# Kernel tuning notes

Measured on AMD Instinct MI355X. Metric: run time of the kernel, lower is better.

## Reference

```python
import jax, jax.numpy as jnp
import numpy as np

D_MODEL = 512
N_HEADS = 8
D_K = D_MODEL // N_HEADS
LN_EPS = 1e-5


def setup_inputs() -> dict:
    key = jax.random.key(0)
    ks = jax.random.split(key, 8)
    B, S, D = 2, 4096, D_MODEL
    # xavier_uniform bound for square [D, D] weight
    bound = float(np.sqrt(6.0 / (D + D)))
    x = jax.random.normal(ks[0], (B, S, D), dtype=jnp.float32)
    w_q = jax.random.uniform(ks[1], (D, D), jnp.float32, -bound, bound)
    w_k = jax.random.uniform(ks[2], (D, D), jnp.float32, -bound, bound)
    w_v = jax.random.uniform(ks[3], (D, D), jnp.float32, -bound, bound)
    # w_o: torch Linear default init (kaiming-uniform-ish); uniform is fine as data
    lim = float(1.0 / np.sqrt(D))
    w_o = jax.random.uniform(ks[4], (D, D), jnp.float32, -lim, lim)
    b_o = jax.random.uniform(ks[5], (D,), jnp.float32, -lim, lim)
    ln_gamma = jnp.ones((D,), jnp.float32)
    ln_beta = jnp.zeros((D,), jnp.float32)
    return {"x": x, "w_q": w_q, "w_k": w_k, "w_v": w_v,
            "w_o": w_o, "b_o": b_o, "ln_gamma": ln_gamma, "ln_beta": ln_beta}


def _layer_norm(x, gamma, beta):
    mu = jnp.mean(x, axis=-1, keepdims=True)
    var = jnp.mean(jnp.square(x - mu), axis=-1, keepdims=True)
    return (x - mu) * jax.lax.rsqrt(var + LN_EPS) * gamma + beta


def reference(x, w_q, w_k, w_v, w_o, b_o, ln_gamma, ln_beta):
    B, S, D = x.shape
    residual = x
    h = _layer_norm(x, ln_gamma, ln_beta)
    # torch Linear: y = h @ W.T ; reshape to [B, H, S, d_k]
    def proj(W):
        return (h @ W.T).reshape(B, S, N_HEADS, D_K).transpose(0, 2, 1, 3)
    Q, K, V = proj(w_q), proj(w_k), proj(w_v)
    scores = jnp.einsum('bhqd,bhkd->bhqk', Q, K) / jnp.sqrt(jnp.float32(D_K))
    attn = jax.nn.softmax(scores, axis=-1)  # dropout p=0 -> identity
    attended = jnp.einsum('bhqk,bhkd->bhqd', attn, V)
    attended = attended.transpose(0, 2, 1, 3).reshape(B, S, D)
    out = attended @ w_o.T + b_o
    return out + residual
```

## Files before the change

kernel.cpp:

```cpp
#include <hip/hip_runtime.h>
#include <hip/hip_bf16.h>
#include <stdint.h>


typedef __bf16 bf16;
typedef __attribute__((ext_vector_type(8))) __bf16 bf16x8;
typedef __attribute__((ext_vector_type(4))) __bf16 bf16x4;
typedef __attribute__((ext_vector_type(4))) float f32x4;
typedef __attribute__((ext_vector_type(4))) unsigned int u32x4;

#define LOG2E 1.44269504088896340736f
#define SW(row, grp) (((row) << 6) + ((((grp) ^ ((row) & 7))) << 3))

__device__ __forceinline__ unsigned int pkbf16(float lo, float hi) {
  return __builtin_amdgcn_perm(__builtin_bit_cast(unsigned int, hi),
                               __builtin_bit_cast(unsigned int, lo),
                               0x07060302u);
}

__global__ __launch_bounds__(256) void ln_kernel(
    const float* __restrict__ x, const float* __restrict__ gamma,
    const float* __restrict__ beta, bf16* __restrict__ h) {
  int wave = threadIdx.x >> 6, lane = threadIdx.x & 63;
  int row = blockIdx.x * 4 + wave;
  const float* xr = x + (size_t)row * 512 + lane * 8;
  f32x4 v0 = *(const f32x4*)xr;
  f32x4 v1 = *(const f32x4*)(xr + 4);
  float f[8], s = 0.f, s2 = 0.f;
#pragma unroll
  for (int i = 0; i < 4; ++i) { f[i] = v0[i]; f[4 + i] = v1[i]; }
#pragma unroll
  for (int i = 0; i < 8; ++i) { s += f[i]; s2 += f[i] * f[i]; }
#pragma unroll
  for (int off = 1; off < 64; off <<= 1) {
    s  += __shfl_xor(s, off, 64);
    s2 += __shfl_xor(s2, off, 64);
  }
  float mu  = s * (1.f / 512.f);
  float var = s2 * (1.f / 512.f) - mu * mu;
  float rstd = rsqrtf(var + 1e-5f);
  f32x4 g0 = *(const f32x4*)(gamma + lane * 8);
  f32x4 g1 = *(const f32x4*)(gamma + lane * 8 + 4);
  f32x4 b0 = *(const f32x4*)(beta + lane * 8);
  f32x4 b1 = *(const f32x4*)(beta + lane * 8 + 4);
  bf16x8 o;
#pragma unroll
  for (int i = 0; i < 4; ++i) {
    o[i]     = (bf16)((f[i]     - mu) * rstd * g0[i] + b0[i]);
    o[4 + i] = (bf16)((f[4 + i] - mu) * rstd * g1[i] + b1[i]);
  }
  *(bf16x8*)(h + (size_t)row * 512 + lane * 8) = o;
}

__global__ __launch_bounds__(256) void qkv_kernel(
    const bf16* __restrict__ h, const float* __restrict__ wq,
    const float* __restrict__ wk, const float* __restrict__ wv,
    bf16* __restrict__ Qg, bf16* __restrict__ Kg, bf16* __restrict__ Vtg) {
  __shared__ bf16 As[128 * 64];
  __shared__ bf16 Bs[128 * 64];
  int tid = threadIdx.x, wave = tid >> 6, lane = tid & 63;
  int wm = wave >> 1, wn = wave & 1, quad = lane >> 4, l15 = lane & 15;
  int mtile = blockIdx.x;
  int wsel = blockIdx.y >> 2;
  int nb = blockIdx.y & 3;
  const float* W = (wsel == 0) ? wq : (wsel == 1 ? wk : wv);
  const bf16*  Abase = h + (size_t)mtile * 128 * 512;
  const float* Bbase = W + (size_t)nb * 128 * 512;
  f32x4 acc[4][4];
#pragma unroll
  for (int i = 0; i < 4; ++i)
#pragma unroll
    for (int j = 0; j < 4; ++j) acc[i][j] = (f32x4){0.f, 0.f, 0.f, 0.f};

  int srow = tid >> 3, grp = tid & 7, scol = grp * 8;
  bf16x8 ar[4];
  f32x4 br0[4], br1[4];
#pragma unroll
  for (int k = 0; k < 4; ++k) {
    int rr = srow + k * 32;
    ar[k]  = *(const bf16x8*)(Abase + (size_t)rr * 512 + scol);
    br0[k] = *(const f32x4*)(Bbase + (size_t)rr * 512 + scol);
    br1[k] = *(const f32x4*)(Bbase + (size_t)rr * 512 + scol + 4);
  }
  for (int k0 = 0; k0 < 512; k0 += 64) {
#pragma unroll
    for (int k = 0; k < 4; ++k) {
      int rr = srow + k * 32;
      int w = SW(rr, grp);
      *(bf16x8*)(As + w) = ar[k];
      bf16x8 wb;
#pragma unroll
      for (int j = 0; j < 4; ++j) { wb[j] = (bf16)br0[k][j]; wb[4 + j] = (bf16)br1[k][j]; }
      *(bf16x8*)(Bs + w) = wb;
    }
    __syncthreads();
    if (k0 < 448) {
#pragma unroll
      for (int k = 0; k < 4; ++k) {
        int rr = srow + k * 32;
        ar[k]  = *(const bf16x8*)(Abase + (size_t)rr * 512 + k0 + 64 + scol);
        br0[k] = *(const f32x4*)(Bbase + (size_t)rr * 512 + k0 + 64 + scol);
        br1[k] = *(const f32x4*)(Bbase + (size_t)rr * 512 + k0 + 64 + scol + 4);
      }
    }
#pragma unroll
    for (int c = 0; c < 2; ++c) {
      bf16x8 af[4], bw[4];
#pragma unroll
      for (int mt = 0; mt < 4; ++mt)
        af[mt] = *(const bf16x8*)(As + SW(wm * 64 + mt * 16 + l15, c * 4 + quad));
#pragma unroll
      for (int nt = 0; nt < 4; ++nt)
        bw[nt] = *(const bf16x8*)(Bs + SW(wn * 64 + nt * 16 + l15, c * 4 + quad));
#pragma unroll
      for (int mt = 0; mt < 4; ++mt)
#pragma unroll
        for (int nt = 0; nt < 4; ++nt)
          acc[mt][nt] = __builtin_amdgcn_mfma_f32_16x16x32_bf16(
              bw[nt], af[mt], acc[mt][nt], 0, 0, 0);
    }
    __syncthreads();
  }
  float qscale = (wsel == 0) ? (0.125f * LOG2E) : 1.0f;
#pragma unroll
  for (int mt = 0; mt < 4; ++mt) {
    int m_g = mtile * 128 + wm * 64 + mt * 16 + l15;
    int b = m_g >> 12, s = m_g & 4095;
#pragma unroll
    for (int nt = 0; nt < 4; ++nt) {
      int n_g = nb * 128 + wn * 64 + nt * 16 + quad * 4;
      int head = n_g >> 6, d = n_g & 63;
      f32x4 a = acc[mt][nt];
      if (wsel < 2) {
        bf16* dst = (wsel == 0 ? Qg : Kg) +
                    ((size_t)((b * 8 + head) * 4096 + s)) * 64 + d;
        bf16x4 pk;
#pragma unroll
        for (int r = 0; r < 4; ++r) pk[r] = (bf16)(a[r] * qscale);
        *(bf16x4*)dst = pk;
      } else {
        bf16* dst = Vtg + ((size_t)((b * 8 + head) * 64 + d)) * 4096 + s;
#pragma unroll
        for (int r = 0; r < 4; ++r) dst[(size_t)r * 4096] = (bf16)a[r];
      }
    }
  }
}

__global__ __launch_bounds__(256, 2) void attn_kernel(
    const bf16* __restrict__ Qg, const bf16* __restrict__ Kg,
    const bf16* __restrict__ Vtg, bf16* __restrict__ Og) {
  __shared__ char smem[64 * 1024];
  bf16* KV = (bf16*)smem;
  float* OL = (float*)smem;
  float* Ll = (float*)(smem + 49152);

  int tid = threadIdx.x, wave = tid >> 6, lane = tid & 63;
  int quad = lane >> 4, l15 = lane & 15;
  int qgrp = wave & 1, khalf = wave >> 1;
  int lin = blockIdx.x;
  int bh = ((lin & 7) << 1) | ((lin >> 3) & 1);
  int q0 = (lin >> 4) * 128;
  int hi = bh & 7, bi = bh >> 3;
  const bf16* Kh  = Kg  + (size_t)bh * 4096 * 64;
  const bf16* Vth = Vtg + (size_t)bh * 64 * 4096;

  bf16x8 qf[4][2];
#pragma unroll
  for (int mt = 0; mt < 4; ++mt)
#pragma unroll
    for (int c = 0; c < 2; ++c)
      qf[mt][c] = *(const bf16x8*)(
          Qg + ((size_t)bh * 4096 + q0 + qgrp * 64 + mt * 16 + l15) * 64 +
          c * 32 + quad * 8);

  f32x4 o_acc[4][4], lacc[4];
#pragma unroll
  for (int mt = 0; mt < 4; ++mt) {
    lacc[mt] = (f32x4){0.f, 0.f, 0.f, 0.f};
#pragma unroll
    for (int nt = 0; nt < 4; ++nt) o_acc[mt][nt] = (f32x4){0.f, 0.f, 0.f, 0.f};
  }
  const u32x4 onesu = {0x3F803F80u, 0x3F803F80u, 0x3F803F80u, 0x3F803F80u};
  const bf16x8 ones8 = __builtin_bit_cast(bf16x8, onesu);

  bf16* sbase = KV + khalf * 8192 + (qgrp ? 4096 : 0);
  bf16x8 sr[8];
  int key0 = khalf * 2048;
#pragma unroll
  for (int i = 0; i < 8; ++i) {
    int e = i * 512 + lane * 8;
    sr[i] = qgrp
        ? *(const bf16x8*)(Vth + (size_t)(e >> 6) * 4096 + key0 + (e & 63))
        : *(const bf16x8*)(Kh + (size_t)key0 * 64 + e);
  }
#pragma unroll
  for (int i = 0; i < 8; ++i) {
    int e = i * 512 + lane * 8;
    *(bf16x8*)(sbase + SW(e >> 6, (e >> 3) & 7)) = sr[i];
  }
#pragma unroll
  for (int i = 0; i < 8; ++i) {
    int e = i * 512 + lane * 8;
    sr[i] = qgrp
        ? *(const bf16x8*)(Vth + (size_t)(e >> 6) * 4096 + key0 + 64 + (e & 63))
        : *(const bf16x8*)(Kh + (size_t)(key0 + 64) * 64 + e);
  }
  __syncthreads();

  for (int kt = 0; kt < 32; ++kt) {
    int cur = kt & 1, nxt = cur ^ 1;
    bf16* Ksw = KV + cur * 16384 + khalf * 8192;
    bf16* Vsw = Ksw + 4096;
    if (kt < 31) {
#pragma unroll
      for (int i = 0; i < 8; ++i) {
        int e = i * 512 + lane * 8;
        *(bf16x8*)(sbase + nxt * 16384 + SW(e >> 6, (e >> 3) & 7)) = sr[i];
      }
    }
    if (kt < 30) {
      int kbase = key0 + (kt + 2) * 64;
#pragma unroll
      for (int i = 0; i < 8; ++i) {
        int e = i * 512 + lane * 8;
        sr[i] = qgrp
            ? *(const bf16x8*)(Vth + (size_t)(e >> 6) * 4096 + kbase + (e & 63))
            : *(const bf16x8*)(Kh + (size_t)kbase * 64 + e);
      }
    }
    bf16x8 kf[8];
#pragma unroll
    for (int kb = 0; kb < 4; ++kb)
#pragma unroll
      for (int c = 0; c < 2; ++c)
        kf[kb * 2 + c] = *(const bf16x8*)(Ksw + SW(kb * 16 + l15, c * 4 + quad));
    bf16x8 vf8[2][4];
#pragma unroll
    for (int pr = 0; pr < 2; ++pr)
#pragma unroll
      for (int nt = 0; nt < 4; ++nt) {
        bf16x4 lo = *(const bf16x4*)(
            &Vsw[SW(nt * 16 + l15, (pr * 2) * 2 + (quad >> 1)) + (quad & 1) * 4]);
        bf16x4 hi4 = *(const bf16x4*)(
            &Vsw[SW(nt * 16 + l15, (pr * 2 + 1) * 2 + (quad >> 1)) + (quad & 1) * 4]);
        bf16x8 v;
#pragma unroll
        for (int j = 0; j < 4; ++j) { v[j] = lo[j]; v[4 + j] = hi4[j]; }
        vf8[pr][nt] = v;
      }
#pragma unroll
    for (int mt = 0; mt < 4; ++mt) {
      f32x4 st[4];
#pragma unroll
      for (int kb = 0; kb < 4; ++kb) st[kb] = (f32x4){0.f, 0.f, 0.f, 0.f};
#pragma unroll
      for (int c = 0; c < 2; ++c)
#pragma unroll
        for (int kb = 0; kb < 4; ++kb)
          st[kb] = __builtin_amdgcn_mfma_f32_16x16x32_bf16(
              kf[kb * 2 + c], qf[mt][c], st[kb], 0, 0, 0);
#pragma unroll
      for (int pr = 0; pr < 2; ++pr) {
        float ea[4], eb[4];
#pragma unroll
        for (int r = 0; r < 4; ++r) {
          ea[r] = __builtin_amdgcn_exp2f(st[pr * 2][r]);
          eb[r] = __builtin_amdgcn_exp2f(st[pr * 2 + 1][r]);
        }
        u32x4 pw = {pkbf16(ea[0], ea[1]), pkbf16(ea[2], ea[3]),
                    pkbf16(eb[0], eb[1]), pkbf16(eb[2], eb[3])};
        bf16x8 pk8 = __builtin_bit_cast(bf16x8, pw);
#pragma unroll
        for (int nt = 0; nt < 4; ++nt)
          o_acc[mt][nt] = __builtin_amdgcn_mfma_f32_16x16x32_bf16(
              vf8[pr][nt], pk8, o_acc[mt][nt], 0, 0, 0);
        lacc[mt] = __builtin_amdgcn_mfma_f32_16x16x32_bf16(
            ones8, pk8, lacc[mt], 0, 0, 0);
      }
    }
    __syncthreads();
  }
  if (khalf == 1) {
    float* dst = OL + qgrp * 4096;
#pragma unroll
    for (int mt = 0; mt < 4; ++mt) {
#pragma unroll
      for (int nt = 0; nt < 4; ++nt) {
        int row = mt * 16 + l15;
        int g = nt * 4 + quad;
        int gs = (g & 8) | ((g ^ row) & 7);
        *(f32x4*)(&dst[row * 64 + gs * 4]) = o_acc[mt][nt];
      }
      if (quad == 0) Ll[qgrp * 64 + mt * 16 + l15] = lacc[mt][0];
    }
  }
  __syncthreads();
  if (khalf == 0) {
    const float* src = OL + qgrp * 4096;
#pragma unroll
    for (int mt = 0; mt < 4; ++mt) {
      float lt = lacc[mt][0] + Ll[qgrp * 64 + mt * 16 + l15];
      float inv = 1.0f / lt;
      int q = q0 + qgrp * 64 + mt * 16 + l15;
#pragma unroll
      for (int nt = 0; nt < 4; ++nt) {
        int row = mt * 16 + l15;
        int g = nt * 4 + quad;
        int gs = (g & 8) | ((g ^ row) & 7);
        f32x4 o = *(const f32x4*)(&src[row * 64 + gs * 4]);
        bf16x4 pk;
#pragma unroll
        for (int r = 0; r < 4; ++r)
          pk[r] = (bf16)((o[r] + o_acc[mt][nt][r]) * inv);
        *(bf16x4*)(&Og[((size_t)bi * 4096 + q) * 512 + hi * 64 + nt * 16 +
                       quad * 4]) = pk;
      }
    }
  }
}

__global__ __launch_bounds__(256) void proj_kernel(
    const bf16* __restrict__ A, const float* __restrict__ Wo,
    const float* __restrict__ bo, const float* __restrict__ x,
    float* __restrict__ out) {
  __shared__ bf16 As[128 * 64];
  __shared__ bf16 Bs[128 * 64];
  int tid = threadIdx.x, wave = tid >> 6, lane = tid & 63;
  int wm = wave >> 1, wn = wave & 1, quad = lane >> 4, l15 = lane & 15;
  int mtile = blockIdx.x, nb = blockIdx.y;
  const bf16*  Abase = A + (size_t)mtile * 128 * 512;
  const float* Bbase = Wo + (size_t)nb * 128 * 512;
  f32x4 acc[4][4];
#pragma unroll
  for (int i = 0; i < 4; ++i)
#pragma unroll
    for (int j = 0; j < 4; ++j) acc[i][j] = (f32x4){0.f, 0.f, 0.f, 0.f};

  int srow = tid >> 3, grp = tid & 7, scol = grp * 8;
  bf16x8 ar[4];
  f32x4 br0[4], br1[4];
#pragma unroll
  for (int k = 0; k < 4; ++k) {
    int rr = srow + k * 32;
    ar[k]  = *(const bf16x8*)(Abase + (size_t)rr * 512 + scol);
    br0[k] = *(const f32x4*)(Bbase + (size_t)rr * 512 + scol);
    br1[k] = *(const f32x4*)(Bbase + (size_t)rr * 512 + scol + 4);
  }
  for (int k0 = 0; k0 < 512; k0 += 64) {
#pragma unroll
    for (int k = 0; k < 4; ++k) {
      int rr = srow + k * 32;
      int w = SW(rr, grp);
      *(bf16x8*)(As + w) = ar[k];
      bf16x8 wb;
#pragma unroll
      for (int j = 0; j < 4; ++j) { wb[j] = (bf16)br0[k][j]; wb[4 + j] = (bf16)br1[k][j]; }
      *(bf16x8*)(Bs + w) = wb;
    }
    __syncthreads();
    if (k0 < 448) {
#pragma unroll
      for (int k = 0; k < 4; ++k) {
        int rr = srow + k * 32;
        ar[k]  = *(const bf16x8*)(Abase + (size_t)rr * 512 + k0 + 64 + scol);
        br0[k] = *(const f32x4*)(Bbase + (size_t)rr * 512 + k0 + 64 + scol);
        br1[k] = *(const f32x4*)(Bbase + (size_t)rr * 512 + k0 + 64 + scol + 4);
      }
    }
#pragma unroll
    for (int c = 0; c < 2; ++c) {
      bf16x8 af[4], bw[4];
#pragma unroll
      for (int mt = 0; mt < 4; ++mt)
        af[mt] = *(const bf16x8*)(As + SW(wm * 64 + mt * 16 + l15, c * 4 + quad));
#pragma unroll
      for (int nt = 0; nt < 4; ++nt)
        bw[nt] = *(const bf16x8*)(Bs + SW(wn * 64 + nt * 16 + l15, c * 4 + quad));
#pragma unroll
      for (int mt = 0; mt < 4; ++mt)
#pragma unroll
        for (int nt = 0; nt < 4; ++nt)
          acc[mt][nt] = __builtin_amdgcn_mfma_f32_16x16x32_bf16(
              bw[nt], af[mt], acc[mt][nt], 0, 0, 0);
    }
    __syncthreads();
  }
#pragma unroll
  for (int mt = 0; mt < 4; ++mt) {
    int m_g = mtile * 128 + wm * 64 + mt * 16 + l15;
#pragma unroll
    for (int nt = 0; nt < 4; ++nt) {
      int n_g = nb * 128 + wn * 64 + nt * 16 + quad * 4;
      f32x4 a = acc[mt][nt];
      f32x4 xr = *(const f32x4*)(x + (size_t)m_g * 512 + n_g);
      f32x4 bb = *(const f32x4*)(bo + n_g);
      f32x4 o;
#pragma unroll
      for (int r = 0; r < 4; ++r)
        o[r] = a[r] + bb[r] + xr[r];
      *(f32x4*)(out + (size_t)m_g * 512 + n_g) = o;
    }
  }
}

extern "C" void kernel_launch(void* const* d_in, const int* in_sizes, int n_in,
                              void* d_out, int out_size, void* d_ws, size_t ws_size,
                              hipStream_t stream) {
  const float* x     = (const float*)d_in[0];
  const float* wq    = (const float*)d_in[1];
  const float* wk    = (const float*)d_in[2];
  const float* wv    = (const float*)d_in[3];
  const float* wo    = (const float*)d_in[4];
  const float* bo    = (const float*)d_in[5];
  const float* gamma = (const float*)d_in[6];
  const float* beta  = (const float*)d_in[7];
  float* out = (float*)d_out;
  char* ws = (char*)d_ws;
  const size_t SZ = (size_t)8192 * 512 * sizeof(bf16);
  bf16* h   = (bf16*)(ws);
  bf16* Ao  = (bf16*)(ws);
  bf16* Qg  = (bf16*)(ws + SZ);
  bf16* Kg  = (bf16*)(ws + 2 * SZ);
  bf16* Vtg = (bf16*)(ws + 3 * SZ);

  ln_kernel<<<2048, 256, 0, stream>>>(x, gamma, beta, h);
  qkv_kernel<<<dim3(64, 12), 256, 0, stream>>>(h, wq, wk, wv, Qg, Kg, Vtg);
  attn_kernel<<<512, 256, 0, stream>>>(Qg, Kg, Vtg, Ao);
  proj_kernel<<<dim3(64, 4), 256, 0, stream>>>(Ao, wo, bo, x, out);
}
```

Before: 192.0 us.

## Pre-permute V tile in LDS, add MFMA priority hints, XCD-aware QKV tile order

When V is staged into shared memory it is now written pre-permuted, so the attention loop reads each V fragment with one 16-byte load instead of two 8-byte loads plus a register shuffle. The score MFMAs start from a zero constant instead of a separate zeroing loop, and the MFMA blocks are wrapped in s_setprio to favour matrix issue across waves. The QKV projection grid is remapped so blocks on the same XCD share M-tiles, aiming for better L2 reuse of the activation rows. The tradeoff is more, narrower LDS stores on the V write side.

New measurement: 190.4 us. No clear change (-0.9%).

```diff
diff --git a/kernel.cpp b/kernel.cpp
--- a/kernel.cpp
+++ b/kernel.cpp
@@ -60,9 +60,12 @@
   __shared__ bf16 Bs[128 * 64];
   int tid = threadIdx.x, wave = tid >> 6, lane = tid & 63;
   int wm = wave >> 1, wn = wave & 1, quad = lane >> 4, l15 = lane & 15;
-  int mtile = blockIdx.x;
-  int wsel = blockIdx.y >> 2;
-  int nb = blockIdx.y & 3;
+  int lin = blockIdx.x + (blockIdx.y << 6);
+  int xcd = lin & 7, idx = lin >> 3;
+  int mtile = xcd * 8 + idx / 12;
+  int yy = idx % 12;
+  int wsel = yy >> 2;
+  int nb = yy & 3;
   const float* W = (wsel == 0) ? wq : (wsel == 1 ? wk : wv);
   const bf16*  Abase = h + (size_t)mtile * 128 * 512;
   const float* Bbase = W + (size_t)nb * 128 * 512;
@@ -143,6 +146,29 @@
 #pragma unroll
         for (int r = 0; r < 4; ++r) dst[(size_t)r * 4096] = (bf16)a[r];
       }
+    }
+  }
+}
+
+__device__ __forceinline__ void write_kv_tile(bf16* dst, const bf16x8* sr,
+                                              int qgrp, int lane) {
+  if (!qgrp) {
+#pragma unroll
+    for (int i = 0; i < 8; ++i) {
+      int e = i * 512 + lane * 8;
+      *(bf16x8*)(dst + SW(e >> 6, (e >> 3) & 7)) = sr[i];
+    }
+  } else {
+#pragma unroll
+    for (int i = 0; i < 8; ++i) {
+      int e = i * 512 + lane * 8;
+      int row = e >> 6, g = (e >> 3) & 7;
+      int pr = g >> 2, s = (g >> 1) & 1, gq = g & 1;
+      bf16x4 lo, hi;
+#pragma unroll
+      for (int j = 0; j < 4; ++j) { lo[j] = sr[i][j]; hi[j] = sr[i][4 + j]; }
+      *(bf16x4*)(dst + SW(row, pr * 4 + gq * 2)     + s * 4) = lo;
+      *(bf16x4*)(dst + SW(row, pr * 4 + gq * 2 + 1) + s * 4) = hi;
     }
   }
 }
@@ -183,6 +209,7 @@
   }
   const u32x4 onesu = {0x3F803F80u, 0x3F803F80u, 0x3F803F80u, 0x3F803F80u};
   const bf16x8 ones8 = __builtin_bit_cast(bf16x8, onesu);
+  const f32x4 z4 = {0.f, 0.f, 0.f, 0.f};
 
   bf16* sbase = KV + khalf * 8192 + (qgrp ? 4096 : 0);
   bf16x8 sr[8];
@@ -194,11 +221,7 @@
         ? *(const bf16x8*)(Vth + (size_t)(e >> 6) * 4096 + key0 + (e & 63))
         : *(const bf16x8*)(Kh + (size_t)key0 * 64 + e);
   }
-#pragma unroll
-  for (int i = 0; i < 8; ++i) {
-    int e = i * 512 + lane * 8;
-    *(bf16x8*)(sbase + SW(e >> 6, (e >> 3) & 7)) = sr[i];
-  }
+  write_kv_tile(sbase, sr, qgrp, lane);
 #pragma unroll
   for (int i = 0; i < 8; ++i) {
     int e = i * 512 + lane * 8;
@@ -213,11 +236,7 @@
     bf16* Ksw = KV + cur * 16384 + khalf * 8192;
     bf16* Vsw = Ksw + 4096;
     if (kt < 31) {
-#pragma unroll
-      for (int i = 0; i < 8; ++i) {
-        int e = i * 512 + lane * 8;
-        *(bf16x8*)(sbase + nxt * 16384 + SW(e >> 6, (e >> 3) & 7)) = sr[i];
-      }
+      write_kv_tile(sbase + nxt * 16384, sr, qgrp, lane);
     }
     if (kt < 30) {
       int kbase = key0 + (kt + 2) * 64;
@@ -239,27 +258,21 @@
 #pragma unroll
     for (int pr = 0; pr < 2; ++pr)
 #pragma unroll
-      for (int nt = 0; nt < 4; ++nt) {
-        bf16x4 lo = *(const bf16x4*)(
-            &Vsw[SW(nt * 16 + l15, (pr * 2) * 2 + (quad >> 1)) + (quad & 1) * 4]);
-        bf16x4 hi4 = *(const bf16x4*)(
-            &Vsw[SW(nt * 16 + l15, (pr * 2 + 1) * 2 + (quad >> 1)) + (quad & 1) * 4]);
-        bf16x8 v;
-#pragma unroll
-        for (int j = 0; j < 4; ++j) { v[j] = lo[j]; v[4 + j] = hi4[j]; }
-        vf8[pr][nt] = v;
-      }
+      for (int nt = 0; nt < 4; ++nt)
+        vf8[pr][nt] = *(const bf16x8*)(Vsw + SW(nt * 16 + l15, pr * 4 + quad));
 #pragma unroll
     for (int mt = 0; mt < 4; ++mt) {
       f32x4 st[4];
-#pragma unroll
-      for (int kb = 0; kb < 4; ++kb) st[kb] = (f32x4){0.f, 0.f, 0.f, 0.f};
-#pragma unroll
-      for (int c = 0; c < 2; ++c)
-#pragma unroll
-        for (int kb = 0; kb < 4; ++kb)
-          st[kb] = __builtin_amdgcn_mfma_f32_16x16x32_bf16(
-              kf[kb * 2 + c], qf[mt][c], st[kb], 0, 0, 0);
+      __builtin_amdgcn_s_setprio(1);
+#pragma unroll
+      for (int kb = 0; kb < 4; ++kb)
+        st[kb] = __builtin_amdgcn_mfma_f32_16x16x32_bf16(
+            kf[kb * 2], qf[mt][0], z4, 0, 0, 0);
+#pragma unroll
+      for (int kb = 0; kb < 4; ++kb)
+        st[kb] = __builtin_amdgcn_mfma_f32_16x16x32_bf16(
+            kf[kb * 2 + 1], qf[mt][1], st[kb], 0, 0, 0);
+      __builtin_amdgcn_s_setprio(0);
 #pragma unroll
       for (int pr = 0; pr < 2; ++pr) {
         float ea[4], eb[4];
@@ -271,12 +284,14 @@
         u32x4 pw = {pkbf16(ea[0], ea[1]), pkbf16(ea[2], ea[3]),
                     pkbf16(eb[0], eb[1]), pkbf16(eb[2], eb[3])};
         bf16x8 pk8 = __builtin_bit_cast(bf16x8, pw);
+        __builtin_amdgcn_s_setprio(1);
 #pragma unroll
         for (int nt = 0; nt < 4; ++nt)
           o_acc[mt][nt] = __builtin_amdgcn_mfma_f32_16x16x32_bf16(
               vf8[pr][nt], pk8, o_acc[mt][nt], 0, 0, 0);
         lacc[mt] = __builtin_amdgcn_mfma_f32_16x16x32_bf16(
             ones8, pk8, lacc[mt], 0, 0, 0);
+        __builtin_amdgcn_s_setprio(0);
       }
     }
     __syncthreads();
```
